# Kernel tuning notes

Hardware: AMD Instinct MI355X
Metric: run time of the kernel (lower is better)

## Reference

```python
import jax, jax.numpy as jnp
import numpy as np
import math

B, S, D = 2, 2048, 2048
HQ, HKV = 16, 4            # query heads, kv heads
HD = D // HQ               # head dim = 128
REPS = HQ // HKV           # queries per kv head = 4
KVD = HKV * HD             # 512


def setup_inputs() -> dict:
    key = jax.random.key(0)
    ks = jax.random.split(key, 7)
    s = 0.02
    return {
        "hidden_states": jax.random.normal(ks[0], (B, S, D), dtype=jnp.float32),
        "Wq": jax.random.normal(ks[1], (D, D), dtype=jnp.float32) * s,
        "bq": jnp.zeros((D,), dtype=jnp.float32),
        "Wk": jax.random.normal(ks[2], (D, KVD), dtype=jnp.float32) * s,
        "bk": jnp.zeros((KVD,), dtype=jnp.float32),
        "Wv": jax.random.normal(ks[3], (D, KVD), dtype=jnp.float32) * s,
        "bv": jnp.zeros((KVD,), dtype=jnp.float32),
    }


def reference(hidden_states, Wq, bq, Wk, bk, Wv, bv):
    b, s, d = hidden_states.shape
    # Projections
    q = hidden_states @ Wq + bq                      # [B,S,D]
    k = hidden_states @ Wk + bk                      # [B,S,KVD]
    v = hidden_states @ Wv + bv                      # [B,S,KVD]
    # Split heads. torch repeat_kv_heads uses .repeat (tile), so expanded
    # head h maps to kv head (h mod HKV). Reshape q heads as (REPS, HKV)
    # so axis g indexes the kv head, matching that tiling exactly.
    q = q.reshape(b, s, HQ, HD).transpose(0, 2, 1, 3)          # [B,HQ,S,hd]
    q = q.reshape(b, REPS, HKV, s, HD)                          # [B,R,G,S,hd]
    k = k.reshape(b, s, HKV, HD).transpose(0, 2, 1, 3)          # [B,G,S,hd]
    v = v.reshape(b, s, HKV, HD).transpose(0, 2, 1, 3)          # [B,G,S,hd]
    scale = 1.0 / math.sqrt(HD)
    scores = jnp.einsum('brgsd,bgtd->brgst', q, k) * scale      # [B,R,G,S,S]
    probs = jax.nn.softmax(scores, axis=-1)
    ctx = jnp.einsum('brgst,bgtd->brgsd', probs, v)             # [B,R,G,S,hd]
    ctx = ctx.reshape(b, HQ, s, HD).transpose(0, 2, 1, 3)       # [B,S,HQ,hd]
    return ctx.reshape(b, s, HQ * HD)                            # [B,S,D]
```

## Files before the change

kernel.cpp:

```cpp
#include <hip/hip_runtime.h>
#include <hip/hip_bf16.h>

#define QSCALE   0.08838834764831845f
#define QKSCALE  0.1275174468755322f

typedef __attribute__((ext_vector_type(8))) short bh8;
typedef __attribute__((ext_vector_type(4))) float fx4;
typedef __attribute__((ext_vector_type(4))) short sh4;

typedef const __attribute__((address_space(1))) unsigned GAu;
typedef __attribute__((address_space(3))) unsigned LAu;

__device__ __forceinline__ short f2bf(float f) {
    unsigned u = __float_as_uint(f);
    unsigned r = u + 0x7fffu + ((u >> 16) & 1u);
    return (short)(r >> 16);
}

__device__ __forceinline__ unsigned pk_bf16(float x, float y) {
    union { __hip_bfloat162 h; unsigned u; } cv;
    cv.h = __float22bfloat162_rn(float2{x, y});
    return cv.u;
}

__global__ __launch_bounds__(256) void cvt_x(const float* __restrict__ x,
                                             short* __restrict__ o) {
    int i = blockIdx.x * 256 + threadIdx.x;
    float4 v = ((const float4*)x)[i];
    sh4 s;
    s.x = f2bf(v.x); s.y = f2bf(v.y); s.z = f2bf(v.z); s.w = f2bf(v.w);
    ((sh4*)o)[i] = s;
}

__global__ __launch_bounds__(256) void transpose_w(const float* __restrict__ w,
                                                   short* __restrict__ wt,
                                                   int K, int N) {
    __shared__ float tile[32][33];
    int nb = blockIdx.x, kb = blockIdx.y;
    int tx = threadIdx.x & 31, ty = threadIdx.x >> 5;
#pragma unroll
    for (int j = 0; j < 4; ++j) {
        int k = kb * 32 + ty + j * 8;
        tile[ty + j * 8][tx] = w[(size_t)k * N + nb * 32 + tx];
    }
    __syncthreads();
#pragma unroll
    for (int j = 0; j < 4; ++j) {
        int n = nb * 32 + ty + j * 8;
        wt[(size_t)n * K + kb * 32 + tx] = f2bf(tile[tx][ty + j * 8]);
    }
}

__global__ __launch_bounds__(256) void proj_gemm(
    const short* __restrict__ X,
    const short* __restrict__ WqT,
    const short* __restrict__ WkT,
    const short* __restrict__ WvT,
    const float* __restrict__ bq, const float* __restrict__ bk,
    const float* __restrict__ bv,
    short* __restrict__ Qb, short* __restrict__ Kpk, short* __restrict__ Vpk) {
    __shared__ short As[128 * 32];
    __shared__ short Bs[128 * 32];

    const int tid = threadIdx.x;
    const int bm = blockIdx.x;
    const int ntg = blockIdx.y;

    const short* Wm; const float* bias; int col0, kind;
    if (ntg < 16)      { Wm = WqT; bias = bq; col0 = ntg * 128;        kind = 0; }
    else if (ntg < 20) { Wm = WkT; bias = bk; col0 = (ntg - 16) * 128; kind = 1; }
    else               { Wm = WvT; bias = bv; col0 = (ntg - 20) * 128; kind = 2; }

    const int w = tid >> 6, lane = tid & 63, quad = lane >> 4, l16 = lane & 15;

    fx4 acc[2][8];
#pragma unroll
    for (int i = 0; i < 2; ++i)
#pragma unroll
        for (int j = 0; j < 8; ++j) acc[i][j] = fx4{0.f, 0.f, 0.f, 0.f};

    const int srow = w * 16 + (lane >> 2);
    const int scol = (((lane & 3) ^ ((lane >> 2) & 3)) * 8);
    const short* Ag = X + (size_t)(bm * 128 + srow) * 2048 + scol;
    const short* Bg = Wm + (size_t)(col0 + srow) * 2048 + scol;
    short* AsW = As + w * 512;
    short* BsW = Bs + w * 512;

    const int fchunk = (quad ^ (l16 & 3)) * 8;
    const short* afp0 = As + (w * 32 + l16) * 32 + fchunk;
    const short* afp1 = As + (w * 32 + 16 + l16) * 32 + fchunk;

    for (int kt = 0; kt < 64; ++kt) {
        const int k0 = kt * 32;
        __syncthreads();
#pragma unroll
        for (int j = 0; j < 2; ++j) {
            __builtin_amdgcn_global_load_lds((GAu*)(Ag + (size_t)(j * 64) * 2048 + k0),
                                             (LAu*)(AsW + j * 2048), 16, 0, 0);
            __builtin_amdgcn_global_load_lds((GAu*)(Bg + (size_t)(j * 64) * 2048 + k0),
                                             (LAu*)(BsW + j * 2048), 16, 0, 0);
        }
        __syncthreads();
        bh8 af0 = *(const bh8*)afp0;
        bh8 af1 = *(const bh8*)afp1;
#pragma unroll
        for (int nt = 0; nt < 8; ++nt) {
            bh8 bf = *(const bh8*)(Bs + (nt * 16 + l16) * 32 + fchunk);
            acc[0][nt] = __builtin_amdgcn_mfma_f32_16x16x32_bf16(af0, bf, acc[0][nt], 0, 0, 0);
            acc[1][nt] = __builtin_amdgcn_mfma_f32_16x16x32_bf16(af1, bf, acc[1][nt], 0, 0, 0);
        }
    }

#pragma unroll
    for (int mt = 0; mt < 2; ++mt) {
        int srow2 = bm * 128 + w * 32 + mt * 16 + quad * 4;
#pragma unroll
        for (int nt = 0; nt < 8; ++nt) {
            int c = col0 + nt * 16 + l16;
            float bval = bias[c];
#pragma unroll
            for (int r = 0; r < 4; ++r) {
                int sg = srow2 + r;
                int b = sg >> 11, s = sg & 2047;
                float v = acc[mt][nt][r] + bval;
                int hd = c & 127;
                if (kind == 0) {
                    v *= QKSCALE;
                    int h = c >> 7;
                    Qb[(((size_t)(b * 16 + h) * 2048 + s) << 7) + hd] = f2bf(v);
                } else if (kind == 1) {
                    int g = c >> 7;
                    int ktt = s >> 6, tl = s & 63;
                    int fnt = tl >> 4, fl16 = tl & 15;
                    int ks = hd >> 5, qd = (hd >> 3) & 3, j = hd & 7;
                    size_t frag = (((size_t)(b * 4 + g) * 32 + ktt) * 16 + fnt * 4 + ks);
                    Kpk[frag * 512 + (qd * 16 + fl16) * 8 + j] = f2bf(v);
                } else {
                    int g = c >> 7;
                    int ktt = s >> 6, tl = s & 63;
                    int ts = tl >> 5, qd = (tl >> 3) & 3, j = tl & 7;
                    int fnt = hd >> 4, fl16 = hd & 15;
                    size_t frag = (((size_t)(b * 4 + g) * 32 + ktt) * 16 + fnt * 2 + ts);
                    Vpk[frag * 512 + (qd * 16 + fl16) * 8 + j] = f2bf(v);
                }
            }
        }
    }
}

__global__ __launch_bounds__(256, 4) void attn(
    const short* __restrict__ Qb,
    const short* __restrict__ Kpk,
    const short* __restrict__ Vpk,
    float* __restrict__ out) {
    __shared__ short Ks[16 * 512];
    __shared__ __align__(16) unsigned Ps[4][16][36];

    const int bid = blockIdx.x;
    const int gb = bid & 7;
    const int rep = (bid >> 3) & 3;
    const int qt = bid >> 5;
    const int b = gb >> 2, g = gb & 3;
    const int h = rep * 4 + g;
    const int tid = threadIdx.x, w = tid >> 6, lane = tid & 63;
    const int quad = lane >> 4, l16 = lane & 15;

    bh8 qf[4];
    {
        int s = qt * 64 + w * 16 + l16;
        const short* qp = Qb + (((size_t)(b * 16 + h) * 2048 + s) << 7);
#pragma unroll
        for (int ks = 0; ks < 4; ++ks)
            qf[ks] = *(const bh8*)(qp + ks * 32 + quad * 8);
    }

    const short* kbase = Kpk + ((size_t)gb * 32) * 8192;
    const short* vbase = Vpk + ((size_t)gb * 32) * 8192 + lane * 8;

    fx4 ctx[8];
#pragma unroll
    for (int j = 0; j < 8; ++j) ctx[j] = fx4{0.f, 0.f, 0.f, 0.f};
    float l_part[4] = {0.f, 0.f, 0.f, 0.f};

    for (int kt = 0; kt < 32; ++kt) {
        const short* kp = kbase + (size_t)kt * 8192;
        const short* vp = vbase + (size_t)kt * 8192;

        __syncthreads();
#pragma unroll
        for (int i = 0; i < 4; ++i) {
            int f = w * 4 + i;
            __builtin_amdgcn_global_load_lds((GAu*)(kp + f * 512 + lane * 8),
                                             (LAu*)(Ks + f * 512), 16, 0, 0);
        }
        __syncthreads();

        bh8 vfA[8];
#pragma unroll
        for (int f = 0; f < 8; ++f)
            vfA[f] = *(const bh8*)(vp + f * 512);

        fx4 sc[4];
#pragma unroll
        for (int j = 0; j < 4; ++j) sc[j] = fx4{0.f, 0.f, 0.f, 0.f};
#pragma unroll
        for (int nt = 0; nt < 4; ++nt) {
#pragma unroll
            for (int ks = 0; ks < 4; ++ks) {
                bh8 kf = *(const bh8*)(Ks + (nt * 4 + ks) * 512 + lane * 8);
                sc[nt] = __builtin_amdgcn_mfma_f32_16x16x32_bf16(qf[ks], kf, sc[nt], 0, 0, 0);
            }
        }

#pragma unroll
        for (int r = 0; r < 4; ++r) {
            float p0 = __builtin_amdgcn_exp2f(sc[0][r]);
            float p1 = __builtin_amdgcn_exp2f(sc[1][r]);
            float p2 = __builtin_amdgcn_exp2f(sc[2][r]);
            float p3 = __builtin_amdgcn_exp2f(sc[3][r]);
            l_part[r] += (p0 + p1) + (p2 + p3);
            int m = quad * 4 + r;
            Ps[w][m][l16]      = pk_bf16(p0, p2);
            Ps[w][m][l16 + 16] = pk_bf16(p1, p3);
        }

        bh8 vfB[8];
#pragma unroll
        for (int f = 0; f < 8; ++f)
            vfB[f] = *(const bh8*)(vp + (f + 8) * 512);

        bh8 pa[2];
        {
            const unsigned* pr = &Ps[w][l16][quad * 8];
            uint4 lo = *(const uint4*)(pr);
            uint4 hi = *(const uint4*)(pr + 4);
            unsigned dw[8] = {lo.x, lo.y, lo.z, lo.w, hi.x, hi.y, hi.z, hi.w};
            unsigned a0[4], a1[4];
#pragma unroll
            for (int j = 0; j < 4; ++j) {
                a0[j] = __builtin_amdgcn_perm(dw[2 * j + 1], dw[2 * j], 0x05040100u);
                a1[j] = __builtin_amdgcn_perm(dw[2 * j + 1], dw[2 * j], 0x07060302u);
            }
            pa[0] = *(const bh8*)a0;
            pa[1] = *(const bh8*)a1;
        }

#pragma unroll
        for (int nt = 0; nt < 4; ++nt) {
            ctx[nt] = __builtin_amdgcn_mfma_f32_16x16x32_bf16(pa[0], vfA[nt * 2], ctx[nt], 0, 0, 0);
            ctx[nt] = __builtin_amdgcn_mfma_f32_16x16x32_bf16(pa[1], vfA[nt * 2 + 1], ctx[nt], 0, 0, 0);
        }
#pragma unroll
        for (int nt = 4; nt < 8; ++nt) {
            ctx[nt] = __builtin_amdgcn_mfma_f32_16x16x32_bf16(pa[0], vfB[(nt - 4) * 2], ctx[nt], 0, 0, 0);
            ctx[nt] = __builtin_amdgcn_mfma_f32_16x16x32_bf16(pa[1], vfB[(nt - 4) * 2 + 1], ctx[nt], 0, 0, 0);
        }
    }

    {
        int srow = qt * 64 + w * 16 + quad * 4;
#pragma unroll
        for (int r = 0; r < 4; ++r) {
            float lsum = l_part[r];
            lsum += __shfl_xor(lsum, 1);
            lsum += __shfl_xor(lsum, 2);
            lsum += __shfl_xor(lsum, 4);
            lsum += __shfl_xor(lsum, 8);
            float inv = 1.f / lsum;
            size_t rowoff = ((size_t)b * 2048 + (srow + r)) * 2048 + h * 128;
#pragma unroll
            for (int nt = 0; nt < 8; ++nt)
                out[rowoff + nt * 16 + l16] = ctx[nt][r] * inv;
        }
    }
}

extern "C" void kernel_launch(void* const* d_in, const int* in_sizes, int n_in,
                              void* d_out, int out_size, void* d_ws, size_t ws_size,
                              hipStream_t stream) {
    const float* hs = (const float*)d_in[0];
    const float* Wq = (const float*)d_in[1];
    const float* bq = (const float*)d_in[2];
    const float* Wk = (const float*)d_in[3];
    const float* bk = (const float*)d_in[4];
    const float* Wv = (const float*)d_in[5];
    const float* bv = (const float*)d_in[6];
    float* out = (float*)d_out;

    char* ws = (char*)d_ws;
    short* Xbf = (short*)(ws);
    short* WqT = (short*)(ws + 16777216);
    short* WkT = (short*)(ws + 25165824);
    short* WvT = (short*)(ws + 27262976);
    short* Qb  = (short*)(ws + 29360128);
    short* Kpk = (short*)(ws + 46137344);
    short* Vpk = (short*)(ws + 50331648);

    cvt_x<<<8192, 256, 0, stream>>>(hs, Xbf);
    transpose_w<<<dim3(64, 64), 256, 0, stream>>>(Wq, WqT, 2048, 2048);
    transpose_w<<<dim3(16, 64), 256, 0, stream>>>(Wk, WkT, 2048, 512);
    transpose_w<<<dim3(16, 64), 256, 0, stream>>>(Wv, WvT, 2048, 512);
    proj_gemm<<<dim3(32, 24), 256, 0, stream>>>(Xbf, WqT, WkT, WvT, bq, bk, bv,
                                                Qb, Kpk, Vpk);
    attn<<<1024, 256, 0, stream>>>(Qb, Kpk, Vpk, out);
}
```

Measured before the change: 307.4 us.

## Double-buffer K tiles in LDS and XOR-swizzle the P staging buffer

K tiles now go into two LDS buffers. The next tile's global-to-LDS load is issued before the current tile is computed, and the two barriers per iteration are cut to one at the end of the loop. This is meant to hide K load latency behind the QK and PV MFMAs. Separately, the P staging array drops its padding (36 to 32 columns) and uses an XOR swizzle to avoid LDS bank conflicts. The cost is double the LDS for K (32 KB instead of 16 KB), which may limit occupancy at 4 blocks per CU, plus a correctness risk around completion of the async LDS load before the single barrier.

```diff
diff --git a/kernel.cpp b/kernel.cpp
--- a/kernel.cpp
+++ b/kernel.cpp
@@ -153,8 +153,8 @@
     const short* __restrict__ Kpk,
     const short* __restrict__ Vpk,
     float* __restrict__ out) {
-    __shared__ short Ks[16 * 512];
-    __shared__ __align__(16) unsigned Ps[4][16][36];
+    __shared__ short Ks[2][16 * 512];
+    __shared__ __align__(16) unsigned Ps[4][16][32];
 
     const int bid = blockIdx.x;
     const int gb = bid & 7;
@@ -182,18 +182,27 @@
     for (int j = 0; j < 8; ++j) ctx[j] = fx4{0.f, 0.f, 0.f, 0.f};
     float l_part[4] = {0.f, 0.f, 0.f, 0.f};
 
+#pragma unroll
+    for (int i = 0; i < 4; ++i) {
+        int f = w * 4 + i;
+        __builtin_amdgcn_global_load_lds((GAu*)(kbase + f * 512 + lane * 8),
+                                         (LAu*)(&Ks[0][f * 512]), 16, 0, 0);
+    }
+    __syncthreads();
+
     for (int kt = 0; kt < 32; ++kt) {
-        const short* kp = kbase + (size_t)kt * 8192;
+        const int cur = kt & 1;
         const short* vp = vbase + (size_t)kt * 8192;
 
-        __syncthreads();
-#pragma unroll
-        for (int i = 0; i < 4; ++i) {
-            int f = w * 4 + i;
-            __builtin_amdgcn_global_load_lds((GAu*)(kp + f * 512 + lane * 8),
-                                             (LAu*)(Ks + f * 512), 16, 0, 0);
-        }
-        __syncthreads();
+        if (kt < 31) {
+            const short* kn = kbase + (size_t)(kt + 1) * 8192;
+#pragma unroll
+            for (int i = 0; i < 4; ++i) {
+                int f = w * 4 + i;
+                __builtin_amdgcn_global_load_lds((GAu*)(kn + f * 512 + lane * 8),
+                                                 (LAu*)(&Ks[cur ^ 1][f * 512]), 16, 0, 0);
+            }
+        }
 
         bh8 vfA[8];
 #pragma unroll
@@ -207,7 +216,7 @@
         for (int nt = 0; nt < 4; ++nt) {
 #pragma unroll
             for (int ks = 0; ks < 4; ++ks) {
-                bh8 kf = *(const bh8*)(Ks + (nt * 4 + ks) * 512 + lane * 8);
+                bh8 kf = *(const bh8*)(&Ks[cur][(nt * 4 + ks) * 512] + lane * 8);
                 sc[nt] = __builtin_amdgcn_mfma_f32_16x16x32_bf16(qf[ks], kf, sc[nt], 0, 0, 0);
             }
         }
@@ -220,8 +229,9 @@
             float p3 = __builtin_amdgcn_exp2f(sc[3][r]);
             l_part[r] += (p0 + p1) + (p2 + p3);
             int m = quad * 4 + r;
-            Ps[w][m][l16]      = pk_bf16(p0, p2);
-            Ps[w][m][l16 + 16] = pk_bf16(p1, p3);
+            int xw = (m & 7) << 2;
+            Ps[w][m][l16 ^ xw]        = pk_bf16(p0, p2);
+            Ps[w][m][(l16 + 16) ^ xw] = pk_bf16(p1, p3);
         }
 
         bh8 vfB[8];
@@ -231,9 +241,10 @@
 
         bh8 pa[2];
         {
-            const unsigned* pr = &Ps[w][l16][quad * 8];
-            uint4 lo = *(const uint4*)(pr);
-            uint4 hi = *(const uint4*)(pr + 4);
+            const unsigned* prow = &Ps[w][l16][0];
+            int xr = (l16 & 7) << 2;
+            uint4 lo = *(const uint4*)(prow + ((quad * 8) ^ xr));
+            uint4 hi = *(const uint4*)(prow + ((quad * 8 + 4) ^ xr));
             unsigned dw[8] = {lo.x, lo.y, lo.z, lo.w, hi.x, hi.y, hi.z, hi.w};
             unsigned a0[4], a1[4];
 #pragma unroll
@@ -255,6 +266,8 @@
             ctx[nt] = __builtin_amdgcn_mfma_f32_16x16x32_bf16(pa[0], vfB[(nt - 4) * 2], ctx[nt], 0, 0, 0);
             ctx[nt] = __builtin_amdgcn_mfma_f32_16x16x32_bf16(pa[1], vfB[(nt - 4) * 2 + 1], ctx[nt], 0, 0, 0);
         }
+
+        __syncthreads();
     }
 
     {
```

After: 296.9 us. 3.4% less time.

## Double-buffer K and V tiles in LDS with half-size key tiles

Applied to the files above, without the earlier changes.

Shrinks the key tile from 64 to 32 keys and double-buffers both K and V in LDS via async global_load_lds, prefetching the next tile while the current one is computed. V fragments are now read from shared memory instead of directly from global memory into registers. This aims to hide global load latency and cut register pressure. In exchange it doubles the number of iterations and barriers, and uses more LDS per block, which may reduce occupancy.

```diff
diff --git a/kernel.cpp b/kernel.cpp
--- a/kernel.cpp
+++ b/kernel.cpp
@@ -153,8 +153,9 @@
     const short* __restrict__ Kpk,
     const short* __restrict__ Vpk,
     float* __restrict__ out) {
-    __shared__ short Ks[16 * 512];
-    __shared__ __align__(16) unsigned Ps[4][16][36];
+    __shared__ short Ks[2][8 * 512];
+    __shared__ short Vs[2][8 * 512];
+    __shared__ __align__(16) unsigned Ps[4][16][20];
 
     const int bid = blockIdx.x;
     const int gb = bid & 7;
@@ -175,40 +176,49 @@
     }
 
     const short* kbase = Kpk + ((size_t)gb * 32) * 8192;
-    const short* vbase = Vpk + ((size_t)gb * 32) * 8192 + lane * 8;
+    const short* vbase = Vpk + ((size_t)gb * 32) * 8192;
 
     fx4 ctx[8];
 #pragma unroll
     for (int j = 0; j < 8; ++j) ctx[j] = fx4{0.f, 0.f, 0.f, 0.f};
     float l_part[4] = {0.f, 0.f, 0.f, 0.f};
 
-    for (int kt = 0; kt < 32; ++kt) {
-        const short* kp = kbase + (size_t)kt * 8192;
-        const short* vp = vbase + (size_t)kt * 8192;
-
-        __syncthreads();
-#pragma unroll
-        for (int i = 0; i < 4; ++i) {
-            int f = w * 4 + i;
-            __builtin_amdgcn_global_load_lds((GAu*)(kp + f * 512 + lane * 8),
-                                             (LAu*)(Ks + f * 512), 16, 0, 0);
-        }
-        __syncthreads();
-
-        bh8 vfA[8];
-#pragma unroll
-        for (int f = 0; f < 8; ++f)
-            vfA[f] = *(const bh8*)(vp + f * 512);
-
-        fx4 sc[4];
-#pragma unroll
-        for (int j = 0; j < 4; ++j) sc[j] = fx4{0.f, 0.f, 0.f, 0.f};
-#pragma unroll
-        for (int nt = 0; nt < 4; ++nt) {
+#pragma unroll
+    for (int i = 0; i < 2; ++i) {
+        int f = w * 2 + i;
+        __builtin_amdgcn_global_load_lds((GAu*)(kbase + f * 512 + lane * 8),
+                                         (LAu*)(&Ks[0][f * 512]), 16, 0, 0);
+        __builtin_amdgcn_global_load_lds((GAu*)(vbase + (size_t)f * 1024 + lane * 8),
+                                         (LAu*)(&Vs[0][f * 512]), 16, 0, 0);
+    }
+    __syncthreads();
+
+    for (int kt = 0; kt < 64; ++kt) {
+        const int cur = kt & 1;
+
+        if (kt < 63) {
+            const int kn = kt + 1;
+            const short* kp = kbase + (size_t)kn * 4096;
+            const short* vp = vbase + (size_t)(kn >> 1) * 8192 + (kn & 1) * 512;
+#pragma unroll
+            for (int i = 0; i < 2; ++i) {
+                int f = w * 2 + i;
+                __builtin_amdgcn_global_load_lds((GAu*)(kp + f * 512 + lane * 8),
+                                                 (LAu*)(&Ks[cur ^ 1][f * 512]), 16, 0, 0);
+                __builtin_amdgcn_global_load_lds((GAu*)(vp + (size_t)f * 1024 + lane * 8),
+                                                 (LAu*)(&Vs[cur ^ 1][f * 512]), 16, 0, 0);
+            }
+        }
+
+        fx4 sc[2];
+        sc[0] = fx4{0.f, 0.f, 0.f, 0.f};
+        sc[1] = fx4{0.f, 0.f, 0.f, 0.f};
+#pragma unroll
+        for (int nti = 0; nti < 2; ++nti) {
 #pragma unroll
             for (int ks = 0; ks < 4; ++ks) {
-                bh8 kf = *(const bh8*)(Ks + (nt * 4 + ks) * 512 + lane * 8);
-                sc[nt] = __builtin_amdgcn_mfma_f32_16x16x32_bf16(qf[ks], kf, sc[nt], 0, 0, 0);
+                bh8 kf = *(const bh8*)(&Ks[cur][(nti * 4 + ks) * 512] + lane * 8);
+                sc[nti] = __builtin_amdgcn_mfma_f32_16x16x32_bf16(qf[ks], kf, sc[nti], 0, 0, 0);
             }
         }
 
@@ -216,45 +226,31 @@
         for (int r = 0; r < 4; ++r) {
             float p0 = __builtin_amdgcn_exp2f(sc[0][r]);
             float p1 = __builtin_amdgcn_exp2f(sc[1][r]);
-            float p2 = __builtin_amdgcn_exp2f(sc[2][r]);
-            float p3 = __builtin_amdgcn_exp2f(sc[3][r]);
-            l_part[r] += (p0 + p1) + (p2 + p3);
-            int m = quad * 4 + r;
-            Ps[w][m][l16]      = pk_bf16(p0, p2);
-            Ps[w][m][l16 + 16] = pk_bf16(p1, p3);
-        }
-
-        bh8 vfB[8];
-#pragma unroll
-        for (int f = 0; f < 8; ++f)
-            vfB[f] = *(const bh8*)(vp + (f + 8) * 512);
-
-        bh8 pa[2];
+            l_part[r] += p0 + p1;
+            Ps[w][quad * 4 + r][l16] = pk_bf16(p0, p1);
+        }
+
+        bh8 pa;
         {
-            const unsigned* pr = &Ps[w][l16][quad * 8];
-            uint4 lo = *(const uint4*)(pr);
-            uint4 hi = *(const uint4*)(pr + 4);
+            const unsigned* prow = &Ps[w][l16][(quad & 1) * 8];
+            uint4 lo = *(const uint4*)(prow);
+            uint4 hi = *(const uint4*)(prow + 4);
             unsigned dw[8] = {lo.x, lo.y, lo.z, lo.w, hi.x, hi.y, hi.z, hi.w};
-            unsigned a0[4], a1[4];
-#pragma unroll
-            for (int j = 0; j < 4; ++j) {
-                a0[j] = __builtin_amdgcn_perm(dw[2 * j + 1], dw[2 * j], 0x05040100u);
-                a1[j] = __builtin_amdgcn_perm(dw[2 * j + 1], dw[2 * j], 0x07060302u);
-            }
-            pa[0] = *(const bh8*)a0;
-            pa[1] = *(const bh8*)a1;
-        }
-
-#pragma unroll
-        for (int nt = 0; nt < 4; ++nt) {
-            ctx[nt] = __builtin_amdgcn_mfma_f32_16x16x32_bf16(pa[0], vfA[nt * 2], ctx[nt], 0, 0, 0);
-            ctx[nt] = __builtin_amdgcn_mfma_f32_16x16x32_bf16(pa[1], vfA[nt * 2 + 1], ctx[nt], 0, 0, 0);
-        }
-#pragma unroll
-        for (int nt = 4; nt < 8; ++nt) {
-            ctx[nt] = __builtin_amdgcn_mfma_f32_16x16x32_bf16(pa[0], vfB[(nt - 4) * 2], ctx[nt], 0, 0, 0);
-            ctx[nt] = __builtin_amdgcn_mfma_f32_16x16x32_bf16(pa[1], vfB[(nt - 4) * 2 + 1], ctx[nt], 0, 0, 0);
-        }
+            unsigned sel = (quad & 2) ? 0x07060302u : 0x05040100u;
+            unsigned a[4];
+#pragma unroll
+            for (int j = 0; j < 4; ++j)
+                a[j] = __builtin_amdgcn_perm(dw[2 * j + 1], dw[2 * j], sel);
+            pa = *(const bh8*)a;
+        }
+
+#pragma unroll
+        for (int nt = 0; nt < 8; ++nt) {
+            bh8 vf = *(const bh8*)(&Vs[cur][nt * 512] + lane * 8);
+            ctx[nt] = __builtin_amdgcn_mfma_f32_16x16x32_bf16(pa, vf, ctx[nt], 0, 0, 0);
+        }
+
+        __syncthreads();
     }
 
     {
```

Result: faster. 285.6 us (-7.1%).
